# Kernel tuning notes

Hardware: AMD Instinct MI355X
Metric: run time of the kernel (lower is better)

Reference implementation:

```python
import jax, jax.numpy as jnp
import numpy as np

ROPE_FREQ = 100.0

def _rope1d(tok, pos, freq):
    # tok: [B, H, N, D] (D even), pos: [B, N] int positions
    D = tok.shape[-1]
    inv_freq = 1.0 / (freq ** (jnp.arange(0, D, 2, dtype=jnp.float32) / D))  # [D/2]
    ang = pos[:, None, :, None].astype(jnp.float32) * inv_freq  # [B,1,N,D/2]
    cos = jnp.concatenate([jnp.cos(ang), jnp.cos(ang)], axis=-1).astype(tok.dtype)
    sin = jnp.concatenate([jnp.sin(ang), jnp.sin(ang)], axis=-1).astype(tok.dtype)
    x1, x2 = jnp.split(tok, 2, axis=-1)
    rot = jnp.concatenate([-x2, x1], axis=-1)  # rotate_half
    return tok * cos + rot * sin

def _rope2d(tok, pos2d, freq=ROPE_FREQ):
    # tok: [B, H, N, D]; first half of D encodes y (pos2d[...,0]), second half x (pos2d[...,1])
    y, x = jnp.split(tok, 2, axis=-1)
    y = _rope1d(y, pos2d[..., 0], freq)
    x = _rope1d(x, pos2d[..., 1], freq)
    return jnp.concatenate([y, x], axis=-1)

def setup_inputs() -> dict:
    key = jax.random.key(0)
    B, N, D, Hh = 2, 2048, 768, 12
    ks = jax.random.split(key, 8)
    x = jax.random.normal(ks[0], (B, N, D), dtype=jnp.float32)
    pos2d = jax.random.randint(ks[1], (B, N, 2), 0, 64)
    rope_mask = jax.random.randint(ks[2], (B, N), 0, 2).astype(jnp.bool_)
    s = 1.0 / np.sqrt(D)
    qkv_w = jax.random.normal(ks[3], (3 * D, D), dtype=jnp.float32) * s
    qkv_b = jnp.zeros((3 * D,), dtype=jnp.float32)
    proj_w = jax.random.normal(ks[4], (D, D), dtype=jnp.float32) * s
    proj_b = jnp.zeros((D,), dtype=jnp.float32)
    return {"x": x, "qkv_w": qkv_w, "qkv_b": qkv_b, "proj_w": proj_w,
            "proj_b": proj_b, "pos2d": pos2d, "rope_mask": rope_mask}

def reference(x, qkv_w, qkv_b, proj_w, proj_b, pos2d, rope_mask):
    B, N, C = x.shape
    num_heads = 12
    head_dim = C // num_heads
    scale = head_dim ** -0.5
    qkv = x @ qkv_w.T + qkv_b  # [B,N,3C]
    qkv = qkv.reshape(B, N, 3, num_heads, head_dim).transpose(2, 0, 3, 1, 4)
    q, k, v = qkv[0], qkv[1], qkv[2]  # each [B,H,N,hd]
    q_rope = _rope2d(q, pos2d)
    k_rope = _rope2d(k, pos2d)
    mask = rope_mask[:, None, :, None]  # [B,1,N,1]
    q = jnp.where(mask, q_rope, q)
    k = jnp.where(mask, k_rope, k)
    attn = jnp.einsum('bhqd,bhkd->bhqk', q, k) * scale
    attn = jax.nn.softmax(attn, axis=-1)
    out = jnp.einsum('bhqk,bhkd->bhqd', attn, v)
    out = out.transpose(0, 2, 1, 3).reshape(B, N, C)
    out = out @ proj_w.T + proj_b
    return out
```

## Files before the change

kernel.cpp:

```cpp
#include <hip/hip_runtime.h>
#include <stdint.h>

#define B_  2
#define N_  2048
#define C_  768
#define H_  12
#define NT  (B_*N_)
#define C3  (3*C_)

typedef _Float16 h8 __attribute__((ext_vector_type(8)));
typedef _Float16 h4 __attribute__((ext_vector_type(4)));
typedef float    f4 __attribute__((ext_vector_type(4)));
typedef float    f16x __attribute__((ext_vector_type(16)));
typedef uint32_t u4 __attribute__((ext_vector_type(4)));

__device__ __forceinline__ void gload16(const void* g, void* l) {
  __builtin_amdgcn_global_load_lds((const __attribute__((address_space(1))) void*)g,
                                   (__attribute__((address_space(3))) void*)l,
                                   16, 0, 0);
}

__device__ __forceinline__ int xcd_swz(int flat, int nwg) {
  return (flat & 7) * (nwg >> 3) + (flat >> 3);
}

__global__ __launch_bounds__(256) void cvt3(const float* __restrict__ x,
                                            const float* __restrict__ w1,
                                            const float* __restrict__ w2,
                                            _Float16* __restrict__ xo,
                                            _Float16* __restrict__ w1o,
                                            _Float16* __restrict__ w2o) {
  const int NX8  = NT*C_/8;
  const int NW18 = C3*C_/8;
  int c = blockIdx.x*256 + threadIdx.x;
  const float* s; _Float16* d; int off;
  if (c < NX8)            { s = x;  d = xo;  off = c; }
  else if (c < NX8+NW18)  { s = w1; d = w1o; off = c - NX8; }
  else                    { s = w2; d = w2o; off = c - NX8 - NW18; }
  f4 a = *(const f4*)(s + (size_t)off*8);
  f4 b = *(const f4*)(s + (size_t)off*8 + 4);
  h8 o;
#pragma unroll
  for (int j = 0; j < 4; ++j) { o[j] = (_Float16)a[j]; o[j+4] = (_Float16)b[j]; }
  *(h8*)(d + (size_t)off*8) = o;
}

__global__ __launch_bounds__(256) void gemm_qkv(const _Float16* __restrict__ A,
                                                const _Float16* __restrict__ W,
                                                const float* __restrict__ bias,
                                                const int* __restrict__ pos2d,
                                                const void* __restrict__ maskraw,
                                                _Float16* __restrict__ Qd,
                                                _Float16* __restrict__ Kd,
                                                _Float16* __restrict__ Vtd) {
  constexpr int BM = 64, BN = 128, K = C_;
  __shared__ _Float16 Alds[2][BM*32];
  __shared__ _Float16 Wlds[2][BN*32];
  __shared__ int sflags;
  const int tid = threadIdx.x, lane = tid & 63, w = tid >> 6;

  if (tid == 0) sflags = 0;
  __syncthreads();
  const unsigned char* mbytes = (const unsigned char*)maskraw;
  int fl = 0;
#pragma unroll
  for (int k2 = 0; k2 < 16; ++k2) {
    unsigned char v = mbytes[tid*16 + k2];
    if (v == 0x3f) fl |= 1;
    if ((k2 & 3) && v) fl |= 2;
  }
  if (fl) atomicOr(&sflags, fl);

  const int flat = blockIdx.y * gridDim.x + blockIdx.x;
  const int wid  = xcd_swz(flat, gridDim.x * gridDim.y);
  const int bx = wid % gridDim.x, by = wid / gridDim.x;
  const int m0 = by*BM, n0 = bx*BN;
  const int wm = w >> 1, wn = w & 1;
  const int fr = lane & 15, fq = lane >> 4;

  f4 acc[2][4] = {};

  const _Float16* Agp = A + (size_t)(m0 + (tid>>2))*K + (tid&3)*8;
  const _Float16* Wgp0 = W + (size_t)(n0 + (tid>>2))*K + (tid&3)*8;
  const _Float16* Wgp1 = W + (size_t)(n0 + 64 + (tid>>2))*K + (tid&3)*8;

  auto GSTAGE = [&](int buf, int kk) {
    gload16(Agp  + kk, &Alds[buf][(w*64)*8]);
    gload16(Wgp0 + kk, &Wlds[buf][(w*64)*8]);
    gload16(Wgp1 + kk, &Wlds[buf][(256 + w*64)*8]);
  };

  GSTAGE(0, 0);
  int cur = 0;
  for (int kk = 0; kk < K; kk += 32) {
    __syncthreads();
    if (kk + 32 < K) GSTAGE(cur^1, kk + 32);
    h8 af[2], wf[4];
#pragma unroll
    for (int mt = 0; mt < 2; ++mt)
      af[mt] = *(const h8*)&Alds[cur][(wm*32 + mt*16 + fr)*32 + fq*8];
#pragma unroll
    for (int nt = 0; nt < 4; ++nt)
      wf[nt] = *(const h8*)&Wlds[cur][(wn*64 + nt*16 + fr)*32 + fq*8];
#pragma unroll
    for (int mt = 0; mt < 2; ++mt)
#pragma unroll
      for (int nt = 0; nt < 4; ++nt)
        acc[mt][nt] = __builtin_amdgcn_mfma_f32_16x16x32_f16(af[mt], wf[nt], acc[mt][nt], 0, 0, 0);
    cur ^= 1;
  }

  const int cb   = (n0 >> 6) + wn;
  const int matc = cb / 12;
  const int h    = cb % 12;
  const int mode = (sflags & 1) ? 2 : ((sflags & 2) ? 1 : 0);
  float bv[4];
#pragma unroll
  for (int nt = 0; nt < 4; ++nt) bv[nt] = bias[cb*64 + nt*16 + fr];

  if (matc < 2) {
    const float invf = exp2f((float)fr * -0.4152410118f);
    const float sc = (matc == 0) ? 0.1803368801f : 1.0f;
    _Float16* base = (matc == 0) ? Qd : Kd;
#pragma unroll
    for (int mt = 0; mt < 2; ++mt)
#pragma unroll
      for (int j = 0; j < 4; ++j) {
        const int t = m0 + wm*32 + mt*16 + fq*4 + j;
        const int b = t >> 11, n = t & 2047;
        bool msk;
        if (mode == 1)      msk = mbytes[t] != 0;
        else if (mode == 0) msk = ((const int*)maskraw)[t] != 0;
        else                msk = ((const float*)maskraw)[t] != 0.0f;
        const float py = (float)pos2d[t*2 + 0];
        const float px = (float)pos2d[t*2 + 1];
        float sy, cy, sx, cx;
        __sincosf(py * invf, &sy, &cy);
        __sincosf(px * invf, &sx, &cx);
        const float a0 = acc[mt][0][j] + bv[0], a1 = acc[mt][1][j] + bv[1];
        const float a2 = acc[mt][2][j] + bv[2], a3 = acc[mt][3][j] + bv[3];
        const float r0 = msk ? (a0*cy - a1*sy) : a0;
        const float r1 = msk ? (a1*cy + a0*sy) : a1;
        const float r2 = msk ? (a2*cx - a3*sx) : a2;
        const float r3 = msk ? (a3*cx + a2*sx) : a3;
        _Float16* dst = base + ((size_t)(b*H_ + h)*N_ + n)*64;
        dst[fr]      = (_Float16)(r0 * sc);
        dst[fr + 16] = (_Float16)(r1 * sc);
        dst[fr + 32] = (_Float16)(r2 * sc);
        dst[fr + 48] = (_Float16)(r3 * sc);
      }
  } else {
#pragma unroll
    for (int mt = 0; mt < 2; ++mt)
#pragma unroll
      for (int j = 0; j < 4; ++j) {
        const int t = m0 + wm*32 + mt*16 + fq*4 + j;
        const int b = t >> 11, n = t & 2047;
        _Float16* vb = Vtd + (size_t)(b*H_ + h)*64*N_ + n;
#pragma unroll
        for (int nt = 0; nt < 4; ++nt)
          vb[(size_t)(nt*16 + fr)*N_] = (_Float16)(acc[mt][nt][j] + bv[nt]);
      }
  }
}

template<int BM, int BN>
__global__ __launch_bounds__(256) void gemm_bt(const _Float16* __restrict__ A,
                                               const _Float16* __restrict__ W,
                                               const float* __restrict__ bias,
                                               _Float16* __restrict__ Ch,
                                               float* __restrict__ Cf,
                                               int M, int N, int K) {
  __shared__ _Float16 Alds[2][BM*32];
  __shared__ _Float16 Wlds[2][BN*32];
  const int tid = threadIdx.x, lane = tid & 63, w = tid >> 6;
  const int flat = blockIdx.y * gridDim.x + blockIdx.x;
  const int wid  = xcd_swz(flat, gridDim.x * gridDim.y);
  const int bx = wid % gridDim.x, by = wid / gridDim.x;
  const int m0 = by*BM, n0 = bx*BN;
  const int wm = w >> 1, wn = w & 1;
  const int fr = lane & 15, fq = lane >> 4;
  constexpr int MT = BM/32, NTt = BN/32;
  constexpr int AI = (BM*4)/256, WI = (BN*4)/256;

  f4 acc[MT][NTt] = {};

  const _Float16* Agp[AI];
  const _Float16* Wgp[WI];
#pragma unroll
  for (int i = 0; i < AI; ++i) { int c = i*256 + tid; Agp[i] = A + (size_t)(m0 + (c>>2))*K + (c&3)*8; }
#pragma unroll
  for (int i = 0; i < WI; ++i) { int c = i*256 + tid; Wgp[i] = W + (size_t)(n0 + (c>>2))*K + (c&3)*8; }

  auto GSTAGE = [&](int buf, int kk) {
#pragma unroll
    for (int i = 0; i < AI; ++i) gload16(Agp[i] + kk, &Alds[buf][(i*256 + w*64)*8]);
#pragma unroll
    for (int i = 0; i < WI; ++i) gload16(Wgp[i] + kk, &Wlds[buf][(i*256 + w*64)*8]);
  };

  GSTAGE(0, 0);
  int cur = 0;
  for (int kk = 0; kk < K; kk += 32) {
    __syncthreads();
    if (kk + 32 < K) GSTAGE(cur^1, kk + 32);
    h8 af[MT], wf[NTt];
#pragma unroll
    for (int mt = 0; mt < MT; ++mt)
      af[mt] = *(const h8*)&Alds[cur][(wm*(BM/2) + mt*16 + fr)*32 + fq*8];
#pragma unroll
    for (int nt = 0; nt < NTt; ++nt)
      wf[nt] = *(const h8*)&Wlds[cur][(wn*(BN/2) + nt*16 + fr)*32 + fq*8];
#pragma unroll
    for (int mt = 0; mt < MT; ++mt)
#pragma unroll
      for (int nt = 0; nt < NTt; ++nt)
        acc[mt][nt] = __builtin_amdgcn_mfma_f32_16x16x32_f16(af[mt], wf[nt], acc[mt][nt], 0, 0, 0);
    cur ^= 1;
  }

#pragma unroll
  for (int nt = 0; nt < NTt; ++nt) {
    const int col = n0 + wn*(BN/2) + nt*16 + fr;
    const float bv = bias[col];
#pragma unroll
    for (int mt = 0; mt < MT; ++mt) {
      const int row = m0 + wm*(BM/2) + mt*16 + fq*4;
#pragma unroll
      for (int j = 0; j < 4; ++j) {
        const float v = acc[mt][nt][j] + bv;
        if (Ch) Ch[(size_t)(row+j)*N + col] = (_Float16)v;
        else    Cf[(size_t)(row+j)*N + col] = v;
      }
    }
  }
}

#define KSPLIT 2
__global__ __launch_bounds__(256, 3) void attn(const _Float16* __restrict__ Q,
                                               const _Float16* __restrict__ K,
                                               const _Float16* __restrict__ Vt,
                                               _Float16* __restrict__ Opart,
                                               float* __restrict__ lpart) {
  __shared__ _Float16 Klds[2][64*64];
  __shared__ _Float16 Vlds[2][64*64];
  const int tid = threadIdx.x, lane = tid & 63, w = tid >> 6;
  const int q32 = lane & 31;
  const int hi  = lane >> 5;
  const int flat = blockIdx.x + gridDim.x*(blockIdx.y + gridDim.y*blockIdx.z);
  const int wid  = xcd_swz(flat, 16*24*KSPLIT);
  const int qi = wid & 15;
  const int bh = (wid >> 4) % 24;
  const int z  = wid / (16*24);
  const int q0 = qi * 128;
  const int kb0 = z * (N_/KSPLIT), kb1 = kb0 + N_/KSPLIT;
  const _Float16* Qb = Q  + (size_t)bh*N_*64;
  const _Float16* Kb = K  + (size_t)bh*N_*64;
  const _Float16* Vb = Vt + (size_t)bh*64*N_;

  h8 qf[4];
#pragma unroll
  for (int s = 0; s < 4; ++s)
    qf[s] = *(const h8*)&Qb[(size_t)(q0 + w*32 + q32)*64 + s*16 + hi*8];

  f16x o2[2][2];
#pragma unroll
  for (int par = 0; par < 2; ++par)
#pragma unroll
    for (int dg = 0; dg < 2; ++dg)
#pragma unroll
      for (int r = 0; r < 16; ++r) o2[par][dg][r] = 0.f;
  float l_r = 0.f;

  const int sr_l = lane >> 3;
  const int scsw = ((lane & 7) ^ sr_l) * 8;
#define STAGE(buf, kb)                                                          \
  {                                                                             \
    _Float16* kl = &Klds[buf][(w*64)*8];                                        \
    _Float16* vl = &Vlds[buf][(w*64)*8];                                        \
    int r0 = w*8 + sr_l;                                                        \
    gload16(Kb + (size_t)((kb) + r0)*64 + scsw,      kl);                       \
    gload16(Vb + (size_t)r0*N_ + (kb) + scsw,        vl);                       \
    gload16(Kb + (size_t)((kb) + 32 + r0)*64 + scsw, kl + 256*8);               \
    gload16(Vb + (size_t)(32 + r0)*N_ + (kb) + scsw, vl + 256*8);               \
  }

  STAGE(0, kb0);
  int cur = 0;
  const int xr = (q32 & 7) << 3;

  for (int kb = kb0; kb < kb1; kb += 64) {
    __syncthreads();
    if (kb + 64 < kb1) STAGE(cur^1, kb + 64);

#pragma unroll
    for (int kg = 0; kg < 2; ++kg) {
      f16x st;
#pragma unroll
      for (int r = 0; r < 16; ++r) st[r] = -8.65617025f;
      __builtin_amdgcn_s_setprio(1);
#pragma unroll
      for (int s = 0; s < 4; ++s) {
        h8 kf = *(const h8*)&Klds[cur][(kg*32 + q32)*64 + ((s*16 + hi*8) ^ xr)];
        st = __builtin_amdgcn_mfma_f32_32x32x16_f16(kf, qf[s], st, 0, 0, 0);
      }
      __builtin_amdgcn_s_setprio(0);
      float p[16];
      float lacc = 0.f;
#pragma unroll
      for (int r = 0; r < 16; ++r) {
        p[r] = __builtin_amdgcn_exp2f(st[r]);
        lacc += p[r];
      }
      l_r += lacc;
      uint32_t dd[8];
#pragma unroll
      for (int m = 0; m < 8; ++m)
        dd[m] = __builtin_bit_cast(uint32_t, __builtin_amdgcn_cvt_pkrtz(p[2*m], p[2*m+1]));
#pragma unroll
      for (int s16 = 0; s16 < 2; ++s16) {
        uint32_t e0 = dd[4*s16+0], e2 = dd[4*s16+2];
        asm("v_permlane32_swap_b32 %0, %1" : "+v"(e0), "+v"(e2));
        uint32_t e1 = dd[4*s16+1], e3 = dd[4*s16+3];
        asm("v_permlane32_swap_b32 %0, %1" : "+v"(e1), "+v"(e3));
        u4 bb;
        bb[0] = e0; bb[1] = e1; bb[2] = e2; bb[3] = e3;
        h8 pb = __builtin_bit_cast(h8, bb);
        const int kcol = kg*32 + s16*16 + hi*8;
        __builtin_amdgcn_s_setprio(1);
#pragma unroll
        for (int dg = 0; dg < 2; ++dg) {
          h8 vf = *(const h8*)&Vlds[cur][(dg*32 + q32)*64 + (kcol ^ xr)];
          o2[s16][dg] = __builtin_amdgcn_mfma_f32_32x32x16_f16(vf, pb, o2[s16][dg], 0, 0, 0);
        }
        __builtin_amdgcn_s_setprio(0);
      }
    }
    cur ^= 1;
  }

  l_r += __shfl_xor(l_r, 32);

  _Float16* Ob = Opart + ((size_t)z*24 + bh)*N_*64;
  float*    lb = lpart + ((size_t)z*24 + bh)*N_;
  const int n = q0 + w*32 + q32;
  if (hi == 0) lb[n] = l_r;
#pragma unroll
  for (int dg = 0; dg < 2; ++dg)
#pragma unroll
    for (int rq = 0; rq < 4; ++rq) {
      h4 ov;
#pragma unroll
      for (int j = 0; j < 4; ++j)
        ov[j] = (_Float16)(o2[0][dg][rq*4 + j] + o2[1][dg][rq*4 + j]);
      *(h4*)&Ob[(size_t)n*64 + dg*32 + rq*8 + hi*4] = ov;
    }
}

__global__ __launch_bounds__(256) void combine(const _Float16* __restrict__ Opart,
                                               const float* __restrict__ lpart,
                                               _Float16* __restrict__ AO) {
  const int g  = blockIdx.x*256 + threadIdx.x;
  const int d8 = g & 7;
  const int n  = (g >> 3) & 2047;
  const int bh = g >> 14;
  const int b = bh / H_, h = bh % H_;
  const size_t r  = ((size_t)bh*N_ + n);
  const size_t sp = (size_t)24*N_;
  f4 osum[2] = {};
  float l = 0.f;
#pragma unroll
  for (int z = 0; z < KSPLIT; ++z) {
    h8 oz = *(const h8*)&Opart[(r + z*sp)*64 + d8*8];
#pragma unroll
    for (int j = 0; j < 4; ++j) { osum[0][j] += (float)oz[j]; osum[1][j] += (float)oz[j+4]; }
    l += lpart[r + z*sp];
  }
  const float inv = 1.0f / l;
  h8 rr;
#pragma unroll
  for (int j = 0; j < 4; ++j) {
    rr[j]   = (_Float16)(osum[0][j] * inv);
    rr[j+4] = (_Float16)(osum[1][j] * inv);
  }
  *(h8*)&AO[((size_t)b*N_ + n)*C_ + h*64 + d8*8] = rr;
}

extern "C" void kernel_launch(void* const* d_in, const int* in_sizes, int n_in,
                              void* d_out, int out_size, void* d_ws, size_t ws_size,
                              hipStream_t stream) {
  (void)in_sizes; (void)n_in; (void)out_size; (void)ws_size;
  const float* x      = (const float*)d_in[0];
  const float* qkv_w  = (const float*)d_in[1];
  const float* qkv_b  = (const float*)d_in[2];
  const float* proj_w = (const float*)d_in[3];
  const float* proj_b = (const float*)d_in[4];
  const int*   pos2d  = (const int*)d_in[5];
  const void*  rmask  = d_in[6];
  float* out = (float*)d_out;
  char* ws = (char*)d_ws;

  _Float16* Wqh   = (_Float16*)(ws + 0);
  _Float16* Wph   = (_Float16*)(ws + 3538944);
  _Float16* Kh    = (_Float16*)(ws + 4718592);
  _Float16* Vth   = (_Float16*)(ws + 11010048);
  _Float16* Xh    = (_Float16*)(ws + 17301504);
  _Float16* Qh    = (_Float16*)(ws + 23592960);
  _Float16* Opart = (_Float16*)(ws + 29884416);
  float*    lpart = (float*)(ws + 42467328);
  _Float16* AOh   = (_Float16*)(ws + 43253760);

  cvt3<<<2688, 256, 0, stream>>>(x, qkv_w, proj_w, Xh, Wqh, Wph);
  gemm_qkv<<<dim3(C3/128, NT/64), 256, 0, stream>>>(Xh, Wqh, qkv_b, pos2d, rmask, Qh, Kh, Vth);
  attn<<<dim3(N_/128, B_*H_, KSPLIT), 256, 0, stream>>>(Qh, Kh, Vth, Opart, lpart);
  combine<<<(24*N_*8)/256, 256, 0, stream>>>(Opart, lpart, AOh);
  gemm_bt<64,64><<<dim3(C_/64, NT/64), 256, 0, stream>>>(AOh, Wph, proj_b, nullptr, out, NT, C_, C_);
}
```

Measured before the change: 101.9 us.

## Triple-buffer LDS staging with partial vmcnt waits in GEMMs and attention

Moves the QKV GEMM, the generic GEMM and the attention kernel from double-buffered to triple-buffered LDS staging. Two tiles are prefetched up front, and each iteration waits only until the older tile's loads have landed (s_waitcnt vmcnt with the count of newer outstanding loads), then barriers. This keeps two global-to-LDS loads in flight behind the MFMA work instead of draining all loads every step. The cost is more LDS per block, which can reduce occupancy, and a fragile dependence on exact per-thread load counts, which the static_assert guards only for gemm_bt.

```diff
diff --git a/kernel.cpp b/kernel.cpp
--- a/kernel.cpp
+++ b/kernel.cpp
@@ -19,6 +19,14 @@
                                    (__attribute__((address_space(3))) void*)l,
                                    16, 0, 0);
 }
+
+#define WAITBAR(N)                                                      \
+  {                                                                     \
+    asm volatile("s_waitcnt vmcnt(" #N ") lgkmcnt(0)" ::: "memory");    \
+    __builtin_amdgcn_sched_barrier(0);                                  \
+    __builtin_amdgcn_s_barrier();                                       \
+    __builtin_amdgcn_sched_barrier(0);                                  \
+  }
 
 __device__ __forceinline__ int xcd_swz(int flat, int nwg) {
   return (flat & 7) * (nwg >> 3) + (flat >> 3);
@@ -54,8 +62,8 @@
                                                 _Float16* __restrict__ Kd,
                                                 _Float16* __restrict__ Vtd) {
   constexpr int BM = 64, BN = 128, K = C_;
-  __shared__ _Float16 Alds[2][BM*32];
-  __shared__ _Float16 Wlds[2][BN*32];
+  __shared__ _Float16 Alds[3][BM*32];
+  __shared__ _Float16 Wlds[3][BN*32];
   __shared__ int sflags;
   const int tid = threadIdx.x, lane = tid & 63, w = tid >> 6;
 
@@ -91,10 +99,15 @@
   };
 
   GSTAGE(0, 0);
+  GSTAGE(1, 32);
   int cur = 0;
   for (int kk = 0; kk < K; kk += 32) {
-    __syncthreads();
-    if (kk + 32 < K) GSTAGE(cur^1, kk + 32);
+    if (kk + 32 < K) WAITBAR(3)
+    else             WAITBAR(0)
+    if (kk + 64 < K) {
+      int nb = cur + 2; if (nb >= 3) nb -= 3;
+      GSTAGE(nb, kk + 64);
+    }
     h8 af[2], wf[4];
 #pragma unroll
     for (int mt = 0; mt < 2; ++mt)
@@ -107,7 +120,7 @@
 #pragma unroll
       for (int nt = 0; nt < 4; ++nt)
         acc[mt][nt] = __builtin_amdgcn_mfma_f32_16x16x32_f16(af[mt], wf[nt], acc[mt][nt], 0, 0, 0);
-    cur ^= 1;
+    ++cur; if (cur >= 3) cur = 0;
   }
 
   const int cb   = (n0 >> 6) + wn;
@@ -171,8 +184,8 @@
                                                _Float16* __restrict__ Ch,
                                                float* __restrict__ Cf,
                                                int M, int N, int K) {
-  __shared__ _Float16 Alds[2][BM*32];
-  __shared__ _Float16 Wlds[2][BN*32];
+  __shared__ _Float16 Alds[3][BM*32];
+  __shared__ _Float16 Wlds[3][BN*32];
   const int tid = threadIdx.x, lane = tid & 63, w = tid >> 6;
   const int flat = blockIdx.y * gridDim.x + blockIdx.x;
   const int wid  = xcd_swz(flat, gridDim.x * gridDim.y);
@@ -182,6 +195,7 @@
   const int fr = lane & 15, fq = lane >> 4;
   constexpr int MT = BM/32, NTt = BN/32;
   constexpr int AI = (BM*4)/256, WI = (BN*4)/256;
+  static_assert(AI + WI == 2, "this T4 port assumes 2 loads/tile (BM=BN=64)");
 
   f4 acc[MT][NTt] = {};
 
@@ -200,10 +214,15 @@
   };
 
   GSTAGE(0, 0);
+  GSTAGE(1, 32);
   int cur = 0;
   for (int kk = 0; kk < K; kk += 32) {
-    __syncthreads();
-    if (kk + 32 < K) GSTAGE(cur^1, kk + 32);
+    if (kk + 32 < K) WAITBAR(2)
+    else             WAITBAR(0)
+    if (kk + 64 < K) {
+      int nb = cur + 2; if (nb >= 3) nb -= 3;
+      GSTAGE(nb, kk + 64);
+    }
     h8 af[MT], wf[NTt];
 #pragma unroll
     for (int mt = 0; mt < MT; ++mt)
@@ -216,7 +235,7 @@
 #pragma unroll
       for (int nt = 0; nt < NTt; ++nt)
         acc[mt][nt] = __builtin_amdgcn_mfma_f32_16x16x32_f16(af[mt], wf[nt], acc[mt][nt], 0, 0, 0);
-    cur ^= 1;
+    ++cur; if (cur >= 3) cur = 0;
   }
 
 #pragma unroll
@@ -242,8 +261,8 @@
                                                const _Float16* __restrict__ Vt,
                                                _Float16* __restrict__ Opart,
                                                float* __restrict__ lpart) {
-  __shared__ _Float16 Klds[2][64*64];
-  __shared__ _Float16 Vlds[2][64*64];
+  __shared__ _Float16 Klds[3][64*64];
+  __shared__ _Float16 Vlds[3][64*64];
   const int tid = threadIdx.x, lane = tid & 63, w = tid >> 6;
   const int q32 = lane & 31;
   const int hi  = lane >> 5;
@@ -286,12 +305,17 @@
   }
 
   STAGE(0, kb0);
+  STAGE(1, kb0 + 64);
   int cur = 0;
   const int xr = (q32 & 7) << 3;
 
   for (int kb = kb0; kb < kb1; kb += 64) {
-    __syncthreads();
-    if (kb + 64 < kb1) STAGE(cur^1, kb + 64);
+    if (kb + 64 < kb1) WAITBAR(4)
+    else               WAITBAR(0)
+    if (kb + 128 < kb1) {
+      int nb = cur + 2; if (nb >= 3) nb -= 3;
+      STAGE(nb, kb + 128);
+    }
 
 #pragma unroll
     for (int kg = 0; kg < 2; ++kg) {
@@ -336,7 +360,7 @@
         __builtin_amdgcn_s_setprio(0);
       }
     }
-    cur ^= 1;
+    ++cur; if (cur >= 3) cur = 0;
   }
 
   l_r += __shfl_xor(l_r, 32);
```

Measured after the change: 107.0 us. 5.1% more time.
